# Kernel tuning notes

Hardware: AMD Instinct MI355X
Metric: run time of the kernel (lower is better)

## Reference

```python
import jax, jax.numpy as jnp
import numpy as np

B, T, IN, H, J = 64, 512, 16, 512, 8


def setup_inputs() -> dict:
    key = jax.random.key(0)
    ks = jax.random.split(key, 12)
    s = 0.04  # ~1/sqrt(H), matches torch RNN default init scale
    return {
        "x": jax.random.normal(ks[0], (B, T, IN), jnp.float32),
        "W_ih0": s * jax.random.normal(ks[1], (3 * H, IN), jnp.float32),
        "W_hh0": s * jax.random.normal(ks[2], (3 * H, H), jnp.float32),
        "b_ih0": s * jax.random.normal(ks[3], (3 * H,), jnp.float32),
        "b_hh0": s * jax.random.normal(ks[4], (3 * H,), jnp.float32),
        "W_ih1": s * jax.random.normal(ks[5], (3 * H, H), jnp.float32),
        "W_hh1": s * jax.random.normal(ks[6], (3 * H, H), jnp.float32),
        "b_ih1": s * jax.random.normal(ks[7], (3 * H,), jnp.float32),
        "b_hh1": s * jax.random.normal(ks[8], (3 * H,), jnp.float32),
        "fc_W": s * jax.random.normal(ks[9], (2 * J, H), jnp.float32),
        "fc_b": s * jax.random.normal(ks[10], (2 * J,), jnp.float32),
        "h0": jnp.zeros((2, B, H), jnp.float32),
        "theta0": jnp.zeros((B, J), jnp.float32),
        "omega0": jnp.zeros((B, J), jnp.float32),
    }


def _gru_cell(h, xt, Wih, Whh, bih, bhh):
    # torch nn.GRU cell math
    gi = xt @ Wih.T + bih
    gh = h @ Whh.T + bhh
    ir, iz, inn = jnp.split(gi, 3, axis=-1)
    hr, hz, hn = jnp.split(gh, 3, axis=-1)
    r = jax.nn.sigmoid(ir + hr)
    z = jax.nn.sigmoid(iz + hz)
    n = jnp.tanh(inn + r * hn)
    return (1.0 - z) * n + z * h


def reference(x, W_ih0, W_hh0, b_ih0, b_hh0, W_ih1, W_hh1, b_ih1, b_hh1,
              fc_W, fc_b, h0, theta0, omega0):
    # bilinear muscle / joint constants (bilinearInit)
    K0, K1, L0m, L1m, M = 100.0, 2000.0, 0.06, 0.006, 0.05
    Ij, Kj, Bj, dt = 0.004, 5.0, 0.3, 1.0 / 60.0
    ma = jnp.array([-M, M], jnp.float32)  # antagonist moment arms
    Bsz = x.shape[0]
    Jn = theta0.shape[1]

    def step(carry, xt):
        h0_, h1_, th, om = carry
        h0_ = _gru_cell(h0_, xt, W_ih0, W_hh0, b_ih0, b_hh0)
        h1_ = _gru_cell(h1_, h0_, W_ih1, W_hh1, b_ih1, b_hh1)
        # activations per joint, 2 antagonist muscles each
        a = jax.nn.sigmoid(h1_ @ fc_W.T + fc_b).reshape(Bsz, Jn, 2)
        Km = K0 + K1 * a                          # bilinear stiffness
        Lm = L0m + L1m * a                        # bilinear rest length
        F = Km * (Lm - ma * th[..., None])        # muscle force [B,J,2]
        tau = jnp.sum(ma * F, axis=-1)            # joint torque [B,J]
        acc = (tau - Kj * th - Bj * om) / Ij
        om = om + dt * acc
        th = th + dt * om
        return (h0_, h1_, th, om), th

    init = (h0[0], h0[1], theta0, omega0)
    xs = jnp.transpose(x, (1, 0, 2))  # [T,B,IN]
    _, ths = jax.lax.scan(step, init, xs)  # [T,B,J]
    return jnp.transpose(ths, (1, 0, 2))  # [B,T,J]
```

## Files before the change

### kernel.cpp

```cpp
#include <hip/hip_runtime.h>
#include <math.h>

#define NWG 256
#define NTH 512

typedef float vf2 __attribute__((ext_vector_type(2)));

__device__ __forceinline__ float cload(const float* p) {
    return __hip_atomic_load(p, __ATOMIC_RELAXED, __HIP_MEMORY_SCOPE_AGENT);
}
__device__ __forceinline__ void cstore(float* p, float v) {
    __hip_atomic_store(p, v, __ATOMIC_RELAXED, __HIP_MEMORY_SCOPE_AGENT);
}
__device__ __forceinline__ vf2 cload2(const float* p) {
    unsigned long long u = __hip_atomic_load((const unsigned long long*)p,
                                             __ATOMIC_RELAXED, __HIP_MEMORY_SCOPE_AGENT);
    vf2 r;
    r.x = __uint_as_float((unsigned)u);
    r.y = __uint_as_float((unsigned)(u >> 32));
    return r;
}
__device__ __forceinline__ void cstore2(float* p, vf2 v) {
    unsigned long long u = ((unsigned long long)__float_as_uint(v.y) << 32)
                         | (unsigned long long)__float_as_uint(v.x);
    __hip_atomic_store((unsigned long long*)p, u,
                       __ATOMIC_RELAXED, __HIP_MEMORY_SCOPE_AGENT);
}

__device__ __forceinline__ void bar_arrive(unsigned* tree, int w, unsigned gen) {
    unsigned p = __hip_atomic_fetch_add(&tree[(w >> 4) * 16], 1u,
                                        __ATOMIC_RELAXED, __HIP_MEMORY_SCOPE_AGENT);
    if (p + 1u == 16u * gen) {
        unsigned q = __hip_atomic_fetch_add(&tree[272], 1u,
                                            __ATOMIC_RELAXED, __HIP_MEMORY_SCOPE_AGENT);
        if (q + 1u == 16u * gen)
            __hip_atomic_store(&tree[288], gen,
                               __ATOMIC_RELAXED, __HIP_MEMORY_SCOPE_AGENT);
    }
}
__device__ __forceinline__ void bar_wait(unsigned* tree, unsigned gen) {
    unsigned f;
    do {
        f = __hip_atomic_load(&tree[288], __ATOMIC_RELAXED, __HIP_MEMORY_SCOPE_AGENT);
        if (f < gen) __builtin_amdgcn_s_sleep(2);
    } while (f < gen);
}

__global__ void k_init(const float* __restrict__ h0in, float* __restrict__ h0buf,
                       float* __restrict__ h1buf, unsigned* __restrict__ bar) {
    int i = blockIdx.x * 256 + threadIdx.x;
    if (i < 32768) {
        int m = i >> 9, k = i & 511;
        h0buf[32768 + ((k >> 1) << 7) + (m << 1) + (k & 1)] = h0in[i];
    } else if (i < 65536) {
        int j = i - 32768;
        int m = j >> 9, k = j & 511;
        h1buf[32768 + ((k >> 1) << 7) + (m << 1) + (k & 1)] = h0in[i];
    } else if (i < 66560) {
        bar[i - 65536] = 0u;
    }
}

__global__ void k_xt(const float* __restrict__ x, float* __restrict__ xT) {
    int i = blockIdx.x * 256 + threadIdx.x;
    if (i < 131072) {
        int mt = i >> 2, q = i & 3;
        int m = mt >> 9, t = mt & 511;
        float4 v = *(const float4*)(x + (size_t)i * 4);
        *(float4*)(xT + ((size_t)t * 64 + m) * 16 + q * 4) = v;
    }
}

__global__ __launch_bounds__(NTH, 2)
void k_fused(const float* __restrict__ xT,
             const float* __restrict__ Wih0, const float* __restrict__ Whh0,
             const float* __restrict__ bih0, const float* __restrict__ bhh0,
             const float* __restrict__ Wih1, const float* __restrict__ Whh1,
             const float* __restrict__ bih1, const float* __restrict__ bhh1,
             const float* __restrict__ fcW, const float* __restrict__ fcb,
             const float* __restrict__ th0, const float* __restrict__ om0,
             float* __restrict__ out,
             float* __restrict__ h0buf, float* __restrict__ h1buf,
             float* __restrict__ apre_g, unsigned* __restrict__ bar)
{
    const int w = blockIdx.x, tid = threadIdx.x;
    const int v = tid >> 6, m = tid & 63;
    const int c0 = w * 2;
    const int vu = __builtin_amdgcn_readfirstlane(v);
    const int ksu = vu * 64;
    unsigned* treeA = bar;
    unsigned* treeB = bar + 320;
    __shared__ float pl[8 * 12 * 64];
    __shared__ float pl2[8 * 64];

    const float* wp0[6]; const float* wpi[6]; const float* wp1[6];
    #pragma unroll
    for (int g = 0; g < 6; ++g) {
        int row = (g >> 1) * 512 + c0 + (g & 1);
        wp0[g] = Whh0 + (size_t)row * 512 + ksu;
        wpi[g] = Wih1 + (size_t)row * 512 + ksu;
        wp1[g] = Whh1 + (size_t)row * 512 + ksu;
    }
    const bool isFC = (w >= 8 && w < 24);
    const float* fcp = fcW + (size_t)(isFC ? (w - 8) : 0) * 512 + ksu;

    vf2 br0 = {0,0}, bz0 = {0,0}, bin0 = {0,0}, bhn0 = {0,0};
    vf2 bi1r = {0,0}, bi1z = {0,0}, bi1n = {0,0};
    vf2 bh1r = {0,0}, bh1z = {0,0}, bh1n = {0,0};
    if (v == 0) {
        #pragma unroll
        for (int j = 0; j < 2; ++j) {
            int c = c0 + j;
            br0[j]  = bih0[c] + bhh0[c];
            bz0[j]  = bih0[512 + c] + bhh0[512 + c];
            bin0[j] = bih0[1024 + c]; bhn0[j] = bhh0[1024 + c];
            bi1r[j] = bih1[c]; bi1z[j] = bih1[512 + c]; bi1n[j] = bih1[1024 + c];
            bh1r[j] = bhh1[c]; bh1z[j] = bhh1[512 + c]; bh1n[j] = bhh1[1024 + c];
        }
    }
    float th = 0.f, om = 0.f, fb0 = 0.f, fb1 = 0.f;
    if (w == 0) {
        th = th0[tid]; om = om0[tid];
        fb0 = fcb[2 * (tid & 7)]; fb1 = fcb[2 * (tid & 7) + 1];
    }
    vf2 gi_r = {0,0}, gi_z = {0,0}, gi_n = {0,0};
    __syncthreads();

    for (int s = 0; s < 515; ++s) {
        const int pw0 = s & 1, pr0 = (s + 1) & 1;
        if (s >= 1) {
            if (tid == 0) bar_wait(treeA, (unsigned)s);
            __syncthreads();
        }
        if (s <= 512) {
            vf2 a01[12];
            #pragma unroll
            for (int g = 0; g < 12; ++g) a01[g] = (vf2){0.f, 0.f};
            #pragma unroll 1
            for (int kb = 0; kb < 4; ++kb) {
                vf2 hb[8];
                const float* hp = h0buf + pr0 * 32768 + (ksu / 2 + kb * 8) * 128 + m * 2;
                #pragma unroll
                for (int i = 0; i < 8; ++i) hb[i] = cload2(hp + i * 128);
                #pragma unroll
                for (int i = 0; i < 8; ++i) {
                    vf2 hv = hb[i];
                    int ko = kb * 16 + i * 2;
                    #pragma unroll
                    for (int g = 0; g < 6; ++g) {
                        a01[g]     += (*(const vf2*)(wp0[g] + ko)) * hv;
                        a01[6 + g] += (*(const vf2*)(wpi[g] + ko)) * hv;
                    }
                }
            }
            #pragma unroll
            for (int g = 0; g < 12; ++g) pl[(v * 12 + g) * 64 + m] = a01[g].x + a01[g].y;
        }
        __syncthreads();
        if (v == 0) {
            if (s <= 511) {
                vf2 hr = {0,0}, hz = {0,0}, hn = {0,0};
                #pragma unroll
                for (int u = 0; u < 8; ++u) {
                    hr.x += pl[(u * 12 + 0) * 64 + m]; hr.y += pl[(u * 12 + 1) * 64 + m];
                    hz.x += pl[(u * 12 + 2) * 64 + m]; hz.y += pl[(u * 12 + 3) * 64 + m];
                    hn.x += pl[(u * 12 + 4) * 64 + m]; hn.y += pl[(u * 12 + 5) * 64 + m];
                }
                const float* xp = xT + ((size_t)s * 64 + m) * 16;
                vf2 ir = {0,0}, iz = {0,0}, in_ = {0,0};
                #pragma unroll
                for (int k = 0; k < 16; ++k) {
                    float xv = xp[k];
                    ir.x  += Wih0[(size_t)(c0) * 16 + k] * xv;
                    ir.y  += Wih0[(size_t)(c0 + 1) * 16 + k] * xv;
                    iz.x  += Wih0[(size_t)(512 + c0) * 16 + k] * xv;
                    iz.y  += Wih0[(size_t)(512 + c0 + 1) * 16 + k] * xv;
                    in_.x += Wih0[(size_t)(1024 + c0) * 16 + k] * xv;
                    in_.y += Wih0[(size_t)(1024 + c0 + 1) * 16 + k] * xv;
                }
                vf2 hold = cload2(&h0buf[pr0 * 32768 + w * 128 + m * 2]);
                vf2 hnew;
                #pragma unroll
                for (int j = 0; j < 2; ++j) {
                    float r = 1.f / (1.f + expf(-(ir[j] + hr[j] + br0[j])));
                    float z = 1.f / (1.f + expf(-(iz[j] + hz[j] + bz0[j])));
                    float n = tanhf(in_[j] + bin0[j] + r * (hn[j] + bhn0[j]));
                    hnew[j] = (1.f - z) * n + z * hold[j];
                }
                cstore2(&h0buf[pw0 * 32768 + w * 128 + m * 2], hnew);
            }
            if (s >= 1 && s <= 512) {
                gi_r = bi1r; gi_z = bi1z; gi_n = bi1n;
                #pragma unroll
                for (int u = 0; u < 8; ++u) {
                    gi_r.x += pl[(u * 12 + 6) * 64 + m];  gi_r.y += pl[(u * 12 + 7) * 64 + m];
                    gi_z.x += pl[(u * 12 + 8) * 64 + m];  gi_z.y += pl[(u * 12 + 9) * 64 + m];
                    gi_n.x += pl[(u * 12 + 10) * 64 + m]; gi_n.y += pl[(u * 12 + 11) * 64 + m];
                }
            }
        }
        __syncthreads();
        if (tid == 0) {
            bar_arrive(treeA, w, (unsigned)(s + 1));
            bar_wait(treeB, (unsigned)s);
        }
        __syncthreads();
        if (w == 0 && s >= 3) {
            int mc = tid >> 3, j = tid & 7;
            const float* ap = apre_g + ((s + 1) & 1) * 1024;
            float a0 = 1.f / (1.f + expf(-(cload(&ap[(2 * j) * 64 + mc]) + fb0)));
            float a1 = 1.f / (1.f + expf(-(cload(&ap[(2 * j + 1) * 64 + mc]) + fb1)));
            float F0 = (100.f + 2000.f * a0) * (0.06f + 0.006f * a0 + 0.05f * th);
            float F1 = (100.f + 2000.f * a1) * (0.06f + 0.006f * a1 - 0.05f * th);
            float tau = 0.05f * (F1 - F0);
            float acc = (tau - 5.f * th - 0.3f * om) * 250.f;
            om += (1.f / 60.f) * acc;
            th += (1.f / 60.f) * om;
            out[((size_t)mc * 512 + (s - 3)) * 8 + j] = th;
        }
        if (s >= 1 && s <= 513) {
            vf2 a2[6];
            #pragma unroll
            for (int g = 0; g < 6; ++g) a2[g] = (vf2){0.f, 0.f};
            vf2 fd = {0.f, 0.f};
            #pragma unroll 1
            for (int kb = 0; kb < 4; ++kb) {
                vf2 hb[8];
                const float* hp = h1buf + (s & 1) * 32768 + (ksu / 2 + kb * 8) * 128 + m * 2;
                #pragma unroll
                for (int i = 0; i < 8; ++i) hb[i] = cload2(hp + i * 128);
                #pragma unroll
                for (int i = 0; i < 8; ++i) {
                    vf2 hv = hb[i];
                    int ko = kb * 16 + i * 2;
                    #pragma unroll
                    for (int g = 0; g < 6; ++g)
                        a2[g] += (*(const vf2*)(wp1[g] + ko)) * hv;
                    fd += (*(const vf2*)(fcp + ko)) * hv;
                }
            }
            if (s <= 512) {
                #pragma unroll
                for (int g = 0; g < 6; ++g) pl[(v * 12 + g) * 64 + m] = a2[g].x + a2[g].y;
            }
            if (isFC && s >= 2) pl2[v * 64 + m] = fd.x + fd.y;
        }
        __syncthreads();
        if (s >= 1 && s <= 512 && v == 0) {
            vf2 hr = {0,0}, hz = {0,0}, hn = {0,0};
            #pragma unroll
            for (int u = 0; u < 8; ++u) {
                hr.x += pl[(u * 12 + 0) * 64 + m]; hr.y += pl[(u * 12 + 1) * 64 + m];
                hz.x += pl[(u * 12 + 2) * 64 + m]; hz.y += pl[(u * 12 + 3) * 64 + m];
                hn.x += pl[(u * 12 + 4) * 64 + m]; hn.y += pl[(u * 12 + 5) * 64 + m];
            }
            vf2 hold = cload2(&h1buf[(s & 1) * 32768 + w * 128 + m * 2]);
            vf2 hnew;
            #pragma unroll
            for (int j = 0; j < 2; ++j) {
                float r = 1.f / (1.f + expf(-(gi_r[j] + hr[j] + bh1r[j])));
                float z = 1.f / (1.f + expf(-(gi_z[j] + hz[j] + bh1z[j])));
                float n = tanhf(gi_n[j] + r * (hn[j] + bh1n[j]));
                hnew[j] = (1.f - z) * n + z * hold[j];
            }
            cstore2(&h1buf[((s + 1) & 1) * 32768 + w * 128 + m * 2], hnew);
        }
        if (isFC && s >= 2 && s <= 513 && v == 2) {
            float p = 0.f;
            #pragma unroll
            for (int u = 0; u < 8; ++u) p += pl2[u * 64 + m];
            cstore(&apre_g[(s & 1) * 1024 + (w - 8) * 64 + m], p);
        }
        if (s == 514) break;
        __syncthreads();
        if (tid == 0) bar_arrive(treeB, w, (unsigned)(s + 1));
    }
}

extern "C" void kernel_launch(void* const* d_in, const int* in_sizes, int n_in,
                              void* d_out, int out_size, void* d_ws, size_t ws_size,
                              hipStream_t stream) {
    const float* x     = (const float*)d_in[0];
    const float* W_ih0 = (const float*)d_in[1];
    const float* W_hh0 = (const float*)d_in[2];
    const float* b_ih0 = (const float*)d_in[3];
    const float* b_hh0 = (const float*)d_in[4];
    const float* W_ih1 = (const float*)d_in[5];
    const float* W_hh1 = (const float*)d_in[6];
    const float* b_ih1 = (const float*)d_in[7];
    const float* b_hh1 = (const float*)d_in[8];
    const float* fc_W  = (const float*)d_in[9];
    const float* fc_b  = (const float*)d_in[10];
    const float* h0    = (const float*)d_in[11];
    const float* th0   = (const float*)d_in[12];
    const float* om0   = (const float*)d_in[13];
    float* out = (float*)d_out;

    float* ws = (float*)d_ws;
    float* h0buf  = ws;
    float* h1buf  = h0buf + 65536;
    float* apre_g = h1buf + 65536;
    unsigned* bar = (unsigned*)(apre_g + 2048);
    float* xT     = (float*)(bar + 1024);

    k_init<<<260, 256, 0, stream>>>(h0, h0buf, h1buf, bar);
    k_xt<<<512, 256, 0, stream>>>(x, xT);

    void* args[] = {(void*)&xT, (void*)&W_ih0, (void*)&W_hh0, (void*)&b_ih0,
                    (void*)&b_hh0, (void*)&W_ih1, (void*)&W_hh1, (void*)&b_ih1,
                    (void*)&b_hh1, (void*)&fc_W, (void*)&fc_b,
                    (void*)&th0, (void*)&om0, (void*)&out, (void*)&h0buf,
                    (void*)&h1buf, (void*)&apre_g, (void*)&bar};
    (void)hipLaunchCooperativeKernel((void*)k_fused, dim3(NWG), dim3(NTH),
                                     args, 0, stream);
}
```

Measured before the change: 5.076 ms.

## Merge two grid barriers per step into one by skewing layer-1 pipeline

Restructures the persistent fused GRU kernel so each time step uses a single grid-wide barrier instead of two. Layer-0 and layer-1 hidden-state matvecs now run in the same phase: layer 1 works on the previous step's layer-0 output while both h0 and h1 slices are loaded up front into registers. Layer-1 gate finalisation moves to wavefront 1 so it runs alongside layer-0 on wavefront 0. The aim is to halve cross-workgroup synchronisation latency per step, at the cost of more register pressure (64 vf2 of preloaded state) and a larger shared-memory scratch area.

```diff
diff --git a/kernel.cpp b/kernel.cpp
--- a/kernel.cpp
+++ b/kernel.cpp
@@ -88,9 +88,7 @@
     const int c0 = w * 2;
     const int vu = __builtin_amdgcn_readfirstlane(v);
     const int ksu = vu * 64;
-    unsigned* treeA = bar;
-    unsigned* treeB = bar + 320;
-    __shared__ float pl[8 * 12 * 64];
+    __shared__ float pl[8 * 18 * 64];
     __shared__ float pl2[8 * 64];
 
     const float* wp0[6]; const float* wpi[6]; const float* wp1[6];
@@ -114,6 +112,12 @@
             br0[j]  = bih0[c] + bhh0[c];
             bz0[j]  = bih0[512 + c] + bhh0[512 + c];
             bin0[j] = bih0[1024 + c]; bhn0[j] = bhh0[1024 + c];
+        }
+    }
+    if (v == 1) {
+        #pragma unroll
+        for (int j = 0; j < 2; ++j) {
+            int c = c0 + j;
             bi1r[j] = bih1[c]; bi1z[j] = bih1[512 + c]; bi1n[j] = bih1[1024 + c];
             bh1r[j] = bhh1[c]; bh1z[j] = bhh1[512 + c]; bh1n[j] = bhh1[1024 + c];
         }
@@ -123,88 +127,14 @@
         th = th0[tid]; om = om0[tid];
         fb0 = fcb[2 * (tid & 7)]; fb1 = fcb[2 * (tid & 7) + 1];
     }
-    vf2 gi_r = {0,0}, gi_z = {0,0}, gi_n = {0,0};
     __syncthreads();
 
     for (int s = 0; s < 515; ++s) {
         const int pw0 = s & 1, pr0 = (s + 1) & 1;
         if (s >= 1) {
-            if (tid == 0) bar_wait(treeA, (unsigned)s);
+            if (tid == 0) bar_wait(bar, (unsigned)s);
             __syncthreads();
         }
-        if (s <= 512) {
-            vf2 a01[12];
-            #pragma unroll
-            for (int g = 0; g < 12; ++g) a01[g] = (vf2){0.f, 0.f};
-            #pragma unroll 1
-            for (int kb = 0; kb < 4; ++kb) {
-                vf2 hb[8];
-                const float* hp = h0buf + pr0 * 32768 + (ksu / 2 + kb * 8) * 128 + m * 2;
-                #pragma unroll
-                for (int i = 0; i < 8; ++i) hb[i] = cload2(hp + i * 128);
-                #pragma unroll
-                for (int i = 0; i < 8; ++i) {
-                    vf2 hv = hb[i];
-                    int ko = kb * 16 + i * 2;
-                    #pragma unroll
-                    for (int g = 0; g < 6; ++g) {
-                        a01[g]     += (*(const vf2*)(wp0[g] + ko)) * hv;
-                        a01[6 + g] += (*(const vf2*)(wpi[g] + ko)) * hv;
-                    }
-                }
-            }
-            #pragma unroll
-            for (int g = 0; g < 12; ++g) pl[(v * 12 + g) * 64 + m] = a01[g].x + a01[g].y;
-        }
-        __syncthreads();
-        if (v == 0) {
-            if (s <= 511) {
-                vf2 hr = {0,0}, hz = {0,0}, hn = {0,0};
-                #pragma unroll
-                for (int u = 0; u < 8; ++u) {
-                    hr.x += pl[(u * 12 + 0) * 64 + m]; hr.y += pl[(u * 12 + 1) * 64 + m];
-                    hz.x += pl[(u * 12 + 2) * 64 + m]; hz.y += pl[(u * 12 + 3) * 64 + m];
-                    hn.x += pl[(u * 12 + 4) * 64 + m]; hn.y += pl[(u * 12 + 5) * 64 + m];
-                }
-                const float* xp = xT + ((size_t)s * 64 + m) * 16;
-                vf2 ir = {0,0}, iz = {0,0}, in_ = {0,0};
-                #pragma unroll
-                for (int k = 0; k < 16; ++k) {
-                    float xv = xp[k];
-                    ir.x  += Wih0[(size_t)(c0) * 16 + k] * xv;
-                    ir.y  += Wih0[(size_t)(c0 + 1) * 16 + k] * xv;
-                    iz.x  += Wih0[(size_t)(512 + c0) * 16 + k] * xv;
-                    iz.y  += Wih0[(size_t)(512 + c0 + 1) * 16 + k] * xv;
-                    in_.x += Wih0[(size_t)(1024 + c0) * 16 + k] * xv;
-                    in_.y += Wih0[(size_t)(1024 + c0 + 1) * 16 + k] * xv;
-                }
-                vf2 hold = cload2(&h0buf[pr0 * 32768 + w * 128 + m * 2]);
-                vf2 hnew;
-                #pragma unroll
-                for (int j = 0; j < 2; ++j) {
-                    float r = 1.f / (1.f + expf(-(ir[j] + hr[j] + br0[j])));
-                    float z = 1.f / (1.f + expf(-(iz[j] + hz[j] + bz0[j])));
-                    float n = tanhf(in_[j] + bin0[j] + r * (hn[j] + bhn0[j]));
-                    hnew[j] = (1.f - z) * n + z * hold[j];
-                }
-                cstore2(&h0buf[pw0 * 32768 + w * 128 + m * 2], hnew);
-            }
-            if (s >= 1 && s <= 512) {
-                gi_r = bi1r; gi_z = bi1z; gi_n = bi1n;
-                #pragma unroll
-                for (int u = 0; u < 8; ++u) {
-                    gi_r.x += pl[(u * 12 + 6) * 64 + m];  gi_r.y += pl[(u * 12 + 7) * 64 + m];
-                    gi_z.x += pl[(u * 12 + 8) * 64 + m];  gi_z.y += pl[(u * 12 + 9) * 64 + m];
-                    gi_n.x += pl[(u * 12 + 10) * 64 + m]; gi_n.y += pl[(u * 12 + 11) * 64 + m];
-                }
-            }
-        }
-        __syncthreads();
-        if (tid == 0) {
-            bar_arrive(treeA, w, (unsigned)(s + 1));
-            bar_wait(treeB, (unsigned)s);
-        }
-        __syncthreads();
         if (w == 0 && s >= 3) {
             int mc = tid >> 3, j = tid & 7;
             const float* ap = apre_g + ((s + 1) & 1) * 1024;
@@ -218,49 +148,107 @@
             th += (1.f / 60.f) * om;
             out[((size_t)mc * 512 + (s - 3)) * 8 + j] = th;
         }
-        if (s >= 1 && s <= 513) {
-            vf2 a2[6];
-            #pragma unroll
-            for (int g = 0; g < 6; ++g) a2[g] = (vf2){0.f, 0.f};
-            vf2 fd = {0.f, 0.f};
-            #pragma unroll 1
-            for (int kb = 0; kb < 4; ++kb) {
-                vf2 hb[8];
-                const float* hp = h1buf + (s & 1) * 32768 + (ksu / 2 + kb * 8) * 128 + m * 2;
-                #pragma unroll
-                for (int i = 0; i < 8; ++i) hb[i] = cload2(hp + i * 128);
-                #pragma unroll
-                for (int i = 0; i < 8; ++i) {
-                    vf2 hv = hb[i];
-                    int ko = kb * 16 + i * 2;
+        {
+            vf2 ha[32], hc[32];
+            const float* hp0 = h0buf + pr0 * 32768 + (ksu >> 1) * 128 + m * 2;
+            const float* hp1 = h1buf + (s & 1) * 32768 + (ksu >> 1) * 128 + m * 2;
+            if (s <= 512) {
+                #pragma unroll
+                for (int i = 0; i < 32; ++i) ha[i] = cload2(hp0 + i * 128);
+            }
+            if (s >= 1 && s <= 513) {
+                #pragma unroll
+                for (int i = 0; i < 32; ++i) hc[i] = cload2(hp1 + i * 128);
+            }
+            if (s <= 512) {
+                vf2 a01[12];
+                #pragma unroll
+                for (int g = 0; g < 12; ++g) a01[g] = (vf2){0.f, 0.f};
+                #pragma unroll
+                for (int i = 0; i < 32; ++i) {
+                    vf2 hv = ha[i];
+                    int ko = i * 2;
+                    #pragma unroll
+                    for (int g = 0; g < 6; ++g) {
+                        a01[g]     += (*(const vf2*)(wp0[g] + ko)) * hv;
+                        a01[6 + g] += (*(const vf2*)(wpi[g] + ko)) * hv;
+                    }
+                }
+                #pragma unroll
+                for (int g = 0; g < 12; ++g)
+                    pl[(v * 18 + g) * 64 + m] = a01[g].x + a01[g].y;
+            }
+            if (s >= 1 && s <= 513) {
+                vf2 a2[6];
+                #pragma unroll
+                for (int g = 0; g < 6; ++g) a2[g] = (vf2){0.f, 0.f};
+                vf2 fd = {0.f, 0.f};
+                #pragma unroll
+                for (int i = 0; i < 32; ++i) {
+                    vf2 hv = hc[i];
+                    int ko = i * 2;
                     #pragma unroll
                     for (int g = 0; g < 6; ++g)
                         a2[g] += (*(const vf2*)(wp1[g] + ko)) * hv;
                     fd += (*(const vf2*)(fcp + ko)) * hv;
                 }
-            }
-            if (s <= 512) {
-                #pragma unroll
-                for (int g = 0; g < 6; ++g) pl[(v * 12 + g) * 64 + m] = a2[g].x + a2[g].y;
-            }
-            if (isFC && s >= 2) pl2[v * 64 + m] = fd.x + fd.y;
+                #pragma unroll
+                for (int g = 0; g < 6; ++g)
+                    pl[(v * 18 + 12 + g) * 64 + m] = a2[g].x + a2[g].y;
+                if (isFC && s >= 2) pl2[v * 64 + m] = fd.x + fd.y;
+            }
         }
         __syncthreads();
-        if (s >= 1 && s <= 512 && v == 0) {
+        if (v == 0 && s <= 511) {
             vf2 hr = {0,0}, hz = {0,0}, hn = {0,0};
             #pragma unroll
             for (int u = 0; u < 8; ++u) {
-                hr.x += pl[(u * 12 + 0) * 64 + m]; hr.y += pl[(u * 12 + 1) * 64 + m];
-                hz.x += pl[(u * 12 + 2) * 64 + m]; hz.y += pl[(u * 12 + 3) * 64 + m];
-                hn.x += pl[(u * 12 + 4) * 64 + m]; hn.y += pl[(u * 12 + 5) * 64 + m];
+                hr.x += pl[(u * 18 + 0) * 64 + m]; hr.y += pl[(u * 18 + 1) * 64 + m];
+                hz.x += pl[(u * 18 + 2) * 64 + m]; hz.y += pl[(u * 18 + 3) * 64 + m];
+                hn.x += pl[(u * 18 + 4) * 64 + m]; hn.y += pl[(u * 18 + 5) * 64 + m];
+            }
+            const float* xp = xT + ((size_t)s * 64 + m) * 16;
+            vf2 ir = {0,0}, iz = {0,0}, in_ = {0,0};
+            #pragma unroll
+            for (int k = 0; k < 16; ++k) {
+                float xv = xp[k];
+                ir.x  += Wih0[(size_t)(c0) * 16 + k] * xv;
+                ir.y  += Wih0[(size_t)(c0 + 1) * 16 + k] * xv;
+                iz.x  += Wih0[(size_t)(512 + c0) * 16 + k] * xv;
+                iz.y  += Wih0[(size_t)(512 + c0 + 1) * 16 + k] * xv;
+                in_.x += Wih0[(size_t)(1024 + c0) * 16 + k] * xv;
+                in_.y += Wih0[(size_t)(1024 + c0 + 1) * 16 + k] * xv;
+            }
+            vf2 hold = cload2(&h0buf[pr0 * 32768 + w * 128 + m * 2]);
+            vf2 hnew;
+            #pragma unroll
+            for (int j = 0; j < 2; ++j) {
+                float r = 1.f / (1.f + expf(-(ir[j] + hr[j] + br0[j])));
+                float z = 1.f / (1.f + expf(-(iz[j] + hz[j] + bz0[j])));
+                float n = tanhf(in_[j] + bin0[j] + r * (hn[j] + bhn0[j]));
+                hnew[j] = (1.f - z) * n + z * hold[j];
+            }
+            cstore2(&h0buf[pw0 * 32768 + w * 128 + m * 2], hnew);
+        }
+        if (v == 1 && s >= 1 && s <= 512) {
+            vf2 gr = bi1r, gz = bi1z, gn = bi1n;
+            vf2 hr = {0,0}, hz = {0,0}, hn = {0,0};
+            #pragma unroll
+            for (int u = 0; u < 8; ++u) {
+                gr.x += pl[(u * 18 + 6) * 64 + m];  gr.y += pl[(u * 18 + 7) * 64 + m];
+                gz.x += pl[(u * 18 + 8) * 64 + m];  gz.y += pl[(u * 18 + 9) * 64 + m];
+                gn.x += pl[(u * 18 + 10) * 64 + m]; gn.y += pl[(u * 18 + 11) * 64 + m];
+                hr.x += pl[(u * 18 + 12) * 64 + m]; hr.y += pl[(u * 18 + 13) * 64 + m];
+                hz.x += pl[(u * 18 + 14) * 64 + m]; hz.y += pl[(u * 18 + 15) * 64 + m];
+                hn.x += pl[(u * 18 + 16) * 64 + m]; hn.y += pl[(u * 18 + 17) * 64 + m];
             }
             vf2 hold = cload2(&h1buf[(s & 1) * 32768 + w * 128 + m * 2]);
             vf2 hnew;
             #pragma unroll
             for (int j = 0; j < 2; ++j) {
-                float r = 1.f / (1.f + expf(-(gi_r[j] + hr[j] + bh1r[j])));
-                float z = 1.f / (1.f + expf(-(gi_z[j] + hz[j] + bh1z[j])));
-                float n = tanhf(gi_n[j] + r * (hn[j] + bh1n[j]));
+                float r = 1.f / (1.f + expf(-(gr[j] + hr[j] + bh1r[j])));
+                float z = 1.f / (1.f + expf(-(gz[j] + hz[j] + bh1z[j])));
+                float n = tanhf(gn[j] + r * (hn[j] + bh1n[j]));
                 hnew[j] = (1.f - z) * n + z * hold[j];
             }
             cstore2(&h1buf[((s + 1) & 1) * 32768 + w * 128 + m * 2], hnew);
@@ -273,7 +261,7 @@
         }
         if (s == 514) break;
         __syncthreads();
-        if (tid == 0) bar_arrive(treeB, w, (unsigned)(s + 1));
+        if (tid == 0) bar_arrive(bar, w, (unsigned)(s + 1));
     }
 }
 
```

Result: slower. 6.213 ms (+22.4%).
